# Kernel optimization log

Hardware: AMD Instinct MI355X
Metric: run time of the kernel (lower is better)

The kernel has to match this reference:

```python
import jax, jax.numpy as jnp
import numpy as np

B, Q, T, C = 2, 300, 25, 256
NH, NL, NP = 8, 4, 4
DFF = 1024
HD = C // NH
SHAPES = [(128, 128), (64, 64), (32, 32), (16, 16)]  # (H_l, W_l) per level
S = sum(h * w for h, w in SHAPES)
LQ = Q * T


def setup_inputs() -> dict:
    key = jax.random.key(0)
    ks = jax.random.split(key, 16)
    rn = lambda k, shape, s=0.02: jax.random.normal(k, shape, jnp.float32) * s
    starts = np.cumsum([0] + [h * w for h, w in SHAPES[:-1]])
    return {
        "tgt_text": jax.random.normal(ks[0], (B, Q, T, C), jnp.float32),
        "query_pos_text": jax.random.normal(ks[1], (B, Q, T, C), jnp.float32),
        "reference_points": jax.random.uniform(ks[2], (B, LQ, NL, 2), jnp.float32),
        "src": jax.random.normal(ks[3], (B, S, C), jnp.float32),
        "src_spatial_shapes": jnp.array(SHAPES, jnp.int32),
        "level_start_index": jnp.array(starts, jnp.int32),
        "in_proj_w": rn(ks[4], (3 * C, C)), "in_proj_b": jnp.zeros((3 * C,), jnp.float32),
        "out_proj_w": rn(ks[5], (C, C)), "out_proj_b": jnp.zeros((C,), jnp.float32),
        "ln1_g": jnp.ones((C,), jnp.float32), "ln1_b": jnp.zeros((C,), jnp.float32),
        "samp_off_w": rn(ks[6], (NH * NL * NP * 2, C)), "samp_off_b": rn(ks[7], (NH * NL * NP * 2,), 0.5),
        "aw_w": rn(ks[8], (NH * NL * NP, C)), "aw_b": jnp.zeros((NH * NL * NP,), jnp.float32),
        "vp_w": rn(ks[9], (C, C)), "vp_b": jnp.zeros((C,), jnp.float32),
        "op_w": rn(ks[10], (C, C)), "op_b": jnp.zeros((C,), jnp.float32),
        "ln2_g": jnp.ones((C,), jnp.float32), "ln2_b": jnp.zeros((C,), jnp.float32),
        "ffn1_w": rn(ks[11], (DFF, C)), "ffn1_b": jnp.zeros((DFF,), jnp.float32),
        "ffn2_w": rn(ks[12], (C, DFF)), "ffn2_b": jnp.zeros((C,), jnp.float32),
        "ln3_g": jnp.ones((C,), jnp.float32), "ln3_b": jnp.zeros((C,), jnp.float32),
    }


def _ln(x, g, b):
    m = jnp.mean(x, axis=-1, keepdims=True)
    v = jnp.var(x, axis=-1, keepdims=True)
    return (x - m) / jnp.sqrt(v + 1e-5) * g + b


def _self_attn(tgt, pos, in_proj_w, in_proj_b, out_proj_w, out_proj_b):
    # torch nn.MultiheadAttention math: q,k carry pos, v is raw tgt
    qk = (tgt + pos).reshape(B * Q, T, C)
    x = tgt.reshape(B * Q, T, C)
    Wq, Wk, Wv = jnp.split(in_proj_w, 3, axis=0)
    bq, bk, bv = jnp.split(in_proj_b, 3, axis=0)
    heads = lambda t: t.reshape(B * Q, T, NH, HD).transpose(0, 2, 1, 3)
    q = heads(qk @ Wq.T + bq)
    k = heads(qk @ Wk.T + bk)
    v = heads(x @ Wv.T + bv)
    attn = jax.nn.softmax(jnp.einsum("bhqd,bhkd->bhqk", q, k) / jnp.sqrt(jnp.float32(HD)), axis=-1)
    o = jnp.einsum("bhqk,bhkd->bhqd", attn, v).transpose(0, 2, 1, 3).reshape(B * Q, T, C)
    return (o @ out_proj_w.T + out_proj_b).reshape(B, Q, T, C)


def _ms_deform_attn(query, reference_points, src, shapes, samp_off_w, samp_off_b, aw_w, aw_b, vp_w, vp_b, op_w, op_b):
    # query: [B, LQ, C]; src: [B, S, C]
    value = (src @ vp_w.T + vp_b).reshape(B, S, NH, HD)
    off = (query @ samp_off_w.T + samp_off_b).reshape(B, LQ, NH, NL, NP, 2)
    aw = jax.nn.softmax((query @ aw_w.T + aw_b).reshape(B, LQ, NH, NL * NP), axis=-1)
    aw = aw.reshape(B, LQ, NH, NL, NP)
    # normalizer is (W_l, H_l)
    norm = jnp.array([[w, h] for (h, w) in shapes], jnp.float32)
    loc = reference_points[:, :, None, :, None, :] + off / norm[None, None, None, :, None, :]
    starts = np.cumsum([0] + [h * w for h, w in shapes])
    accum = jnp.zeros((B, NH, LQ, HD), jnp.float32)
    for l, (Hl, Wl) in enumerate(shapes):
        vl = value[:, starts[l]:starts[l] + Hl * Wl].transpose(0, 2, 1, 3)  # [B,NH,HW,HD]
        # grid_sample align_corners=False pixel coords
        xl = (loc[:, :, :, l, :, 0] * Wl - 0.5).transpose(0, 2, 1, 3).reshape(B, NH, LQ * NP)
        yl = (loc[:, :, :, l, :, 1] * Hl - 0.5).transpose(0, 2, 1, 3).reshape(B, NH, LQ * NP)
        x0 = jnp.floor(xl); y0 = jnp.floor(yl)
        wx1 = xl - x0; wy1 = yl - y0
        x0i = x0.astype(jnp.int32); y0i = y0.astype(jnp.int32)
        samp = jnp.zeros((B, NH, LQ * NP, HD), jnp.float32)
        for dx, dy, w in ((0, 0, (1 - wx1) * (1 - wy1)), (1, 0, wx1 * (1 - wy1)),
                          (0, 1, (1 - wx1) * wy1), (1, 1, wx1 * wy1)):
            xi = x0i + dx; yi = y0i + dy
            valid = (xi >= 0) & (xi < Wl) & (yi >= 0) & (yi < Hl)
            lin = jnp.clip(yi, 0, Hl - 1) * Wl + jnp.clip(xi, 0, Wl - 1)
            g = jnp.take_along_axis(vl, lin[..., None], axis=2)  # [B,NH,LQ*NP,HD]
            samp = samp + g * (w * valid)[..., None]
        samp = samp.reshape(B, NH, LQ, NP, HD)
        awl = aw[:, :, :, l, :].transpose(0, 2, 1, 3)  # [B,NH,LQ,NP]
        accum = accum + jnp.sum(samp * awl[..., None], axis=3)
    out = accum.transpose(0, 2, 1, 3).reshape(B, LQ, C)
    return out @ op_w.T + op_b


def reference(tgt_text, query_pos_text, reference_points, src, src_spatial_shapes, level_start_index,
              in_proj_w, in_proj_b, out_proj_w, out_proj_b, ln1_g, ln1_b,
              samp_off_w, samp_off_b, aw_w, aw_b, vp_w, vp_b, op_w, op_b, ln2_g, ln2_b,
              ffn1_w, ffn1_b, ffn2_w, ffn2_b, ln3_g, ln3_b):
    shapes = [tuple(int(v) for v in row) for row in np.asarray(src_spatial_shapes)]  # static
    # --- intra-text self-attention ---
    tgt2 = _self_attn(tgt_text, query_pos_text, in_proj_w, in_proj_b, out_proj_w, out_proj_b)
    tgt = _ln(tgt_text + tgt2, ln1_g, ln1_b)
    # --- multi-scale deformable cross-attention ---
    query = (tgt + query_pos_text).reshape(B, LQ, C)
    cross = _ms_deform_attn(query, reference_points, src, shapes,
                            samp_off_w, samp_off_b, aw_w, aw_b, vp_w, vp_b, op_w, op_b)
    tgt = _ln(tgt + cross.reshape(B, Q, T, C), ln2_g, ln2_b)
    # --- FFN ---
    ffn = jax.nn.relu(tgt @ ffn1_w.T + ffn1_b) @ ffn2_w.T + ffn2_b
    return _ln(tgt + ffn, ln3_g, ln3_b)
```

## Files before the change

kernel.cpp:

```cpp
#include <hip/hip_runtime.h>
#include <cstddef>

#define B_ 2
#define Q_ 300
#define T_ 25
#define C_ 256
#define NH_ 8
#define NL_ 4
#define NP_ 4
#define HD_ 32
#define DFF_ 1024
#define LQ_ (Q_ * T_)
#define NTOK_ (B_ * LQ_)
#define S_ 21760
#define BS_ (B_ * S_)

typedef __bf16 bf16x8 __attribute__((ext_vector_type(8)));
typedef float floatx4 __attribute__((ext_vector_type(4)));
typedef unsigned short ushort_t;

__device__ __forceinline__ unsigned pack_bf16(float x, float y) {
    unsigned ux = __float_as_uint(x) + 0x8000u;
    unsigned uy = __float_as_uint(y) + 0x8000u;
    return (ux >> 16) | (uy & 0xFFFF0000u);
}
__device__ __forceinline__ ushort_t f2bf_s(float x) {
    return (ushort_t)((__float_as_uint(x) + 0x8000u) >> 16);
}
__device__ __forceinline__ float bf2f(ushort_t u) {
    return __uint_as_float((unsigned)u << 16);
}

#define WOFF_IP   0
#define WOFF_OUT  196608
#define WOFF_VP   262144
#define WOFF_SO   327680
#define WOFF_AW   393216
#define WOFF_OP   425984
#define WOFF_F1   491520
#define WOFF_F2   753664
#define WTOTAL    1015808

__global__ __launch_bounds__(256) void convw_kernel(
    const float* __restrict__ ipw, const float* __restrict__ outw,
    const float* __restrict__ vpw, const float* __restrict__ sampw,
    const float* __restrict__ aww, const float* __restrict__ opw,
    const float* __restrict__ f1w, const float* __restrict__ f2w,
    ushort_t* __restrict__ dst)
{
    long long g = ((long long)blockIdx.x * 256 + threadIdx.x) * 8;
    if (g >= WTOTAL) return;
    const float* src; long long off;
    if      (g < WOFF_OUT) { src = ipw;   off = WOFF_IP; }
    else if (g < WOFF_VP)  { src = outw;  off = WOFF_OUT; }
    else if (g < WOFF_SO)  { src = vpw;   off = WOFF_VP; }
    else if (g < WOFF_AW)  { src = sampw; off = WOFF_SO; }
    else if (g < WOFF_OP)  { src = aww;   off = WOFF_AW; }
    else if (g < WOFF_F1)  { src = opw;   off = WOFF_OP; }
    else if (g < WOFF_F2)  { src = f1w;   off = WOFF_F1; }
    else                   { src = f2w;   off = WOFF_F2; }
    const float4* s4 = (const float4*)(src + (g - off));
    float4 a = s4[0], b = s4[1];
    uint4 o;
    o.x = pack_bf16(a.x, a.y); o.y = pack_bf16(a.z, a.w);
    o.z = pack_bf16(b.x, b.y); o.w = pack_bf16(b.z, b.w);
    *(uint4*)(dst + g) = o;
}

#define GBN 128
#define GBK 32
#define LDA_S 40

template<int AMODE, int OUTMODE, int GBMT>
__global__ __launch_bounds__(256) void gemm_w(
    const void* __restrict__ Av, const float* __restrict__ A2,
    const ushort_t* __restrict__ W,
    const float* __restrict__ bias, const float* __restrict__ bias2, int N1,
    void* __restrict__ Cv, long long partStride,
    int M, int N, int K, int kChunk, int ldc, int relu)
{
    constexpr int LA = GBMT / 32;
    constexpr int WM = GBMT / 2;
    constexpr int NI = WM / 16;

    __shared__ unsigned short Asl[GBMT * LDA_S];
    __shared__ unsigned short Bsl[GBN * LDA_S];

    const int m0 = blockIdx.x * GBMT;
    const int n0 = blockIdx.y * GBN;
    const int z  = blockIdx.z;
    const int kbeg = z * kChunk;
    const int kend = min(K, kbeg + kChunk);

    const int t  = threadIdx.x;
    const int wid  = t >> 6;
    const int lane = t & 63;
    const int wm = (wid >> 1) * WM;
    const int wn = (wid & 1) * 64;
    const int fm = lane & 15;
    const int fq = (lane >> 4) * 8;

    floatx4 acc[NI][4];
    #pragma unroll
    for (int i = 0; i < NI; ++i)
        #pragma unroll
        for (int j = 0; j < 4; ++j)
            acc[i][j] = (floatx4){0.f, 0.f, 0.f, 0.f};

    float4 pa[LA];
    uint2  pab[LA];
    uint2  pwb[4];
    const float* Af = (const float*)Av;
    const ushort_t* Ab = (const ushort_t*)Av;

    auto load_tiles = [&](int k0) {
        #pragma unroll
        for (int i = 0; i < LA; ++i) {
            int idx = t + 256 * i;
            int row = idx >> 3;
            int c4  = (idx & 7) * 4;
            int gm = m0 + row;
            if constexpr (AMODE == 2) {
                uint2 v = {0u, 0u};
                if (gm < M) v = *(const uint2*)(Ab + (size_t)gm * K + k0 + c4);
                pab[i] = v;
            } else {
                float4 v = make_float4(0.f, 0.f, 0.f, 0.f);
                if (gm < M) {
                    v = *(const float4*)(Af + (size_t)gm * K + k0 + c4);
                    if constexpr (AMODE == 1) {
                        float4 v2 = *(const float4*)(A2 + (size_t)gm * K + k0 + c4);
                        v.x += v2.x; v.y += v2.y; v.z += v2.z; v.w += v2.w;
                    }
                }
                pa[i] = v;
            }
        }
        #pragma unroll
        for (int i = 0; i < 4; ++i) {
            int idx = t + 256 * i;
            int row = idx >> 3;
            int c4  = (idx & 7) * 4;
            pwb[i] = *(const uint2*)(W + (size_t)(n0 + row) * K + k0 + c4);
        }
    };

    load_tiles(kbeg);
    for (int k0 = kbeg; k0 < kend; k0 += GBK) {
        #pragma unroll
        for (int i = 0; i < LA; ++i) {
            int idx = t + 256 * i;
            int row = idx >> 3;
            int c4  = (idx & 7) * 4;
            if constexpr (AMODE == 2) {
                *(uint2*)&Asl[row * LDA_S + c4] = pab[i];
            } else {
                uint2 p;
                p.x = pack_bf16(pa[i].x, pa[i].y);
                p.y = pack_bf16(pa[i].z, pa[i].w);
                *(uint2*)&Asl[row * LDA_S + c4] = p;
            }
        }
        #pragma unroll
        for (int i = 0; i < 4; ++i) {
            int idx = t + 256 * i;
            int row = idx >> 3;
            int c4  = (idx & 7) * 4;
            *(uint2*)&Bsl[row * LDA_S + c4] = pwb[i];
        }
        __syncthreads();

        if (k0 + GBK < kend) load_tiles(k0 + GBK);

        bf16x8 af[NI], bfr[4];
        #pragma unroll
        for (int i = 0; i < NI; ++i)
            af[i] = *(const bf16x8*)&Asl[(wm + i * 16 + fm) * LDA_S + fq];
        #pragma unroll
        for (int j = 0; j < 4; ++j)
            bfr[j] = *(const bf16x8*)&Bsl[(wn + j * 16 + fm) * LDA_S + fq];

        #pragma unroll
        for (int i = 0; i < NI; ++i)
            #pragma unroll
            for (int j = 0; j < 4; ++j)
                acc[i][j] = __builtin_amdgcn_mfma_f32_16x16x32_bf16(af[i], bfr[j], acc[i][j], 0, 0, 0);
        __syncthreads();
    }

    float* Cf = (float*)Cv + (long long)z * partStride;
    ushort_t* Cb = (ushort_t*)Cv;
    const int cr = (lane >> 4) * 4;
    const int cc = lane & 15;
    #pragma unroll
    for (int j = 0; j < 4; ++j) {
        int gn = n0 + wn + j * 16 + cc;
        float bia = 0.f;
        if (z == 0) bia = (bias2 && gn >= N1) ? bias2[gn - N1] : bias[gn];
        #pragma unroll
        for (int i = 0; i < NI; ++i) {
            #pragma unroll
            for (int r = 0; r < 4; ++r) {
                int gm = m0 + wm + i * 16 + cr + r;
                if (gm < M) {
                    float v = acc[i][j][r] + bia;
                    if (relu) v = fmaxf(v, 0.f);
                    if constexpr (OUTMODE == 2) {
                        int bb = gm >= S_;
                        int s  = gm - bb * S_;
                        Cb[(((size_t)(bb * 8 + (gn >> 5))) * S_ + s) * 32 + (gn & 31)] = f2bf_s(v);
                    } else if constexpr (OUTMODE == 1) {
                        Cb[(size_t)gm * ldc + gn] = f2bf_s(v);
                    } else {
                        Cf[(size_t)gm * ldc + gn] = v;
                    }
                }
            }
        }
    }
}

__global__ __launch_bounds__(64) void attn_kernel(
    const ushort_t* __restrict__ qkv,
    ushort_t* __restrict__ o)
{
    int sh = blockIdx.x;
    int s = sh >> 3, h = sh & 7;
    __shared__ float qs[T_][HD_], ks[T_][HD_], vs[T_][HD_];
    int t = threadIdx.x;

    for (int idx = t; idx < T_ * HD_; idx += 64) {
        int i = idx >> 5, d = idx & 31;
        size_t base = ((size_t)(s * T_ + i)) * 768 + h * HD_ + d;
        qs[i][d] = bf2f(qkv[base]);
        ks[i][d] = bf2f(qkv[base + 256]);
        vs[i][d] = bf2f(qkv[base + 512]);
    }
    __syncthreads();

    if (t < T_) {
        float sc[T_];
        float mx = -1e30f;
        #pragma unroll
        for (int j = 0; j < T_; ++j) {
            float dot = 0.f;
            #pragma unroll
            for (int d = 0; d < HD_; ++d) dot += qs[t][d] * ks[j][d];
            sc[j] = dot * 0.17677669529663687f;
            mx = fmaxf(mx, sc[j]);
        }
        float sum = 0.f;
        #pragma unroll
        for (int j = 0; j < T_; ++j) { sc[j] = __expf(sc[j] - mx); sum += sc[j]; }
        float inv = 1.f / sum;
        float out[HD_];
        #pragma unroll
        for (int d = 0; d < HD_; ++d) out[d] = 0.f;
        for (int j = 0; j < T_; ++j) {
            float p = sc[j] * inv;
            #pragma unroll
            for (int d = 0; d < HD_; ++d) out[d] += p * vs[j][d];
        }
        size_t ob = ((size_t)(s * T_ + t)) * C_ + h * HD_;
        #pragma unroll
        for (int d = 0; d < HD_; ++d) o[ob + d] = f2bf_s(out[d]);
    }
}

__global__ __launch_bounds__(256) void ln4_kernel(
    const float* __restrict__ x, const float* __restrict__ r,
    int nparts, long long rstride,
    const float* __restrict__ g, const float* __restrict__ b,
    float* __restrict__ out, const float* __restrict__ pos,
    float* __restrict__ qout)
{
    const int wave = threadIdx.x >> 6;
    const int lane = threadIdx.x & 63;
    const int tok = blockIdx.x * 4 + wave;
    const size_t base = (size_t)tok * C_ + lane * 4;

    float4 v = *(const float4*)(x + base);
    for (int p = 0; p < nparts; ++p) {
        float4 rv = *(const float4*)(r + base + (long long)p * rstride);
        v.x += rv.x; v.y += rv.y; v.z += rv.z; v.w += rv.w;
    }
    float s  = v.x + v.y + v.z + v.w;
    float ss = v.x * v.x + v.y * v.y + v.z * v.z + v.w * v.w;
    #pragma unroll
    for (int m = 32; m; m >>= 1) {
        s  += __shfl_xor(s, m);
        ss += __shfl_xor(ss, m);
    }
    float mean = s * (1.f / 256.f);
    float var  = ss * (1.f / 256.f) - mean * mean;
    float rstd = rsqrtf(var + 1e-5f);

    float4 gv = *(const float4*)(g + lane * 4);
    float4 bv = *(const float4*)(b + lane * 4);
    float4 y;
    y.x = (v.x - mean) * rstd * gv.x + bv.x;
    y.y = (v.y - mean) * rstd * gv.y + bv.y;
    y.z = (v.z - mean) * rstd * gv.z + bv.z;
    y.w = (v.w - mean) * rstd * gv.w + bv.w;
    *(float4*)(out + base) = y;
    if (qout) {
        float4 pv = *(const float4*)(pos + base);
        float4 q;
        q.x = y.x + pv.x; q.y = y.y + pv.y; q.z = y.z + pv.z; q.w = y.w + pv.w;
        *(float4*)(qout + base) = q;
    }
}

__global__ __launch_bounds__(256) void deform_kernel(
    const ushort_t* __restrict__ value,
    const float* __restrict__ d12,
    const float* __restrict__ refpts,
    ushort_t* __restrict__ out)
{
    const int lane = threadIdx.x & 63;
    const int wave = threadIdx.x >> 6;
    const int half = lane >> 5;
    const int tok = blockIdx.x * 8 + wave * 2 + half;
    const int h  = (lane >> 2) & 7;
    const int d8 = (lane & 3) * 8;
    const int b = tok / LQ_;

    const float* awp = d12 + (size_t)tok * 384 + 256 + h * 16;
    float logit[16];
    float mx = -1e30f;
    #pragma unroll
    for (int i = 0; i < 16; ++i) { logit[i] = awp[i]; mx = fmaxf(mx, logit[i]); }
    float sum = 0.f;
    #pragma unroll
    for (int i = 0; i < 16; ++i) { logit[i] = __expf(logit[i] - mx); sum += logit[i]; }
    float inv = 1.f / sum;

    const float* offp = d12 + (size_t)tok * 384 + h * 32;
    const float* refp = refpts + (size_t)tok * (NL_ * 2);

    const int HW[4]     = {128, 64, 32, 16};
    const int starts[4] = {0, 16384, 20480, 21504};

    float accv[8];
    #pragma unroll
    for (int i = 0; i < 8; ++i) accv[i] = 0.f;

    #pragma unroll
    for (int l = 0; l < 4; ++l) {
        const int Hl = HW[l], Wl = HW[l];
        float rx = refp[l * 2 + 0], ry = refp[l * 2 + 1];
        const ushort_t* vbase = value + (((size_t)(b * 8 + h)) * S_ + starts[l]) * HD_ + d8;
        #pragma unroll
        for (int p = 0; p < 4; ++p) {
            float ox = offp[(l * 4 + p) * 2 + 0];
            float oy = offp[(l * 4 + p) * 2 + 1];
            float xl = rx * (float)Wl + ox - 0.5f;
            float yl = ry * (float)Hl + oy - 0.5f;
            float x0f = floorf(xl), y0f = floorf(yl);
            int x0 = (int)x0f, y0 = (int)y0f;
            float wx1 = xl - x0f, wy1 = yl - y0f;
            float wx0 = 1.f - wx1, wy0 = 1.f - wy1;
            float aww = logit[l * 4 + p] * inv;

            #pragma unroll
            for (int c = 0; c < 4; ++c) {
                int dx = c & 1, dy = c >> 1;
                int xi = x0 + dx, yi = y0 + dy;
                float w = (dx ? wx1 : wx0) * (dy ? wy1 : wy0);
                bool valid = (xi >= 0) & (xi < Wl) & (yi >= 0) & (yi < Hl);
                int xc = min(max(xi, 0), Wl - 1);
                int yc = min(max(yi, 0), Hl - 1);
                float wc = (valid ? w : 0.f) * aww;
                uint4 raw = *(const uint4*)(vbase + (size_t)(yc * Wl + xc) * HD_);
                accv[0] += __uint_as_float((raw.x & 0xFFFFu) << 16) * wc;
                accv[1] += __uint_as_float(raw.x & 0xFFFF0000u) * wc;
                accv[2] += __uint_as_float((raw.y & 0xFFFFu) << 16) * wc;
                accv[3] += __uint_as_float(raw.y & 0xFFFF0000u) * wc;
                accv[4] += __uint_as_float((raw.z & 0xFFFFu) << 16) * wc;
                accv[5] += __uint_as_float(raw.z & 0xFFFF0000u) * wc;
                accv[6] += __uint_as_float((raw.w & 0xFFFFu) << 16) * wc;
                accv[7] += __uint_as_float(raw.w & 0xFFFF0000u) * wc;
            }
        }
    }
    uint4 po;
    po.x = pack_bf16(accv[0], accv[1]);
    po.y = pack_bf16(accv[2], accv[3]);
    po.z = pack_bf16(accv[4], accv[5]);
    po.w = pack_bf16(accv[6], accv[7]);
    *(uint4*)(out + (size_t)tok * C_ + h * HD_ + d8) = po;
}

extern "C" void kernel_launch(void* const* d_in, const int* in_sizes, int n_in,
                              void* d_out, int out_size, void* d_ws, size_t ws_size,
                              hipStream_t stream) {
    const float* tgt_text = (const float*)d_in[0];
    const float* pos      = (const float*)d_in[1];
    const float* refpts   = (const float*)d_in[2];
    const float* src      = (const float*)d_in[3];
    const float* in_proj_w  = (const float*)d_in[6];
    const float* in_proj_b  = (const float*)d_in[7];
    const float* out_proj_w = (const float*)d_in[8];
    const float* out_proj_b = (const float*)d_in[9];
    const float* ln1_g = (const float*)d_in[10];
    const float* ln1_b = (const float*)d_in[11];
    const float* samp_off_w = (const float*)d_in[12];
    const float* samp_off_b = (const float*)d_in[13];
    const float* aw_w = (const float*)d_in[14];
    const float* aw_b = (const float*)d_in[15];
    const float* vp_w = (const float*)d_in[16];
    const float* vp_b = (const float*)d_in[17];
    const float* op_w = (const float*)d_in[18];
    const float* op_b = (const float*)d_in[19];
    const float* ln2_g = (const float*)d_in[20];
    const float* ln2_b = (const float*)d_in[21];
    const float* ffn1_w = (const float*)d_in[22];
    const float* ffn1_b = (const float*)d_in[23];
    const float* ffn2_w = (const float*)d_in[24];
    const float* ffn2_b = (const float*)d_in[25];
    const float* ln3_g = (const float*)d_in[26];
    const float* ln3_b = (const float*)d_in[27];

    const long long NC = (long long)NTOK_ * C_;
    float* ws = (float*)d_ws;
    float* A    = ws;
    float* Bq   = ws + NC;
    float* Creg = ws + 2 * NC;
    float* D12  = Creg + (long long)NTOK_ * DFF_;
    float* E    = D12 + (long long)NTOK_ * 384;
    float* F    = E + NC;
    ushort_t* wb = (ushort_t*)(F + NC);

    ushort_t* qkv  = (ushort_t*)Creg;
    ushort_t* valt = (ushort_t*)Creg + (size_t)NTOK_ * 768;

    const int MB64  = (NTOK_ + 63) / 64;
    const int MB128 = (NTOK_ + 127) / 128;
    const int MBV64 = BS_ / 64;

    convw_kernel<<<496, 256, 0, stream>>>(in_proj_w, out_proj_w, vp_w, samp_off_w,
                                          aw_w, op_w, ffn1_w, ffn2_w, wb);
    gemm_w<1, 1, 64><<<dim3(MB64, 4, 1), 256, 0, stream>>>(tgt_text, pos, wb + WOFF_IP,
        in_proj_b, nullptr, 0, qkv, 0, NTOK_, 512, 256, 256, 768, 0);
    gemm_w<0, 1, 64><<<dim3(MB64, 2, 1), 256, 0, stream>>>(tgt_text, nullptr, wb + WOFF_IP + 512 * 256,
        in_proj_b + 512, nullptr, 0, qkv + 512, 0, NTOK_, 256, 256, 256, 768, 0);
    gemm_w<0, 2, 64><<<dim3(MBV64, 2, 1), 256, 0, stream>>>(src, nullptr, wb + WOFF_VP,
        vp_b, nullptr, 0, valt, 0, BS_, 256, 256, 256, 0, 0);
    attn_kernel<<<B_ * Q_ * NH_, 64, 0, stream>>>(qkv, (ushort_t*)E);
    gemm_w<2, 0, 64><<<dim3(MB64, 2, 1), 256, 0, stream>>>(E, nullptr, wb + WOFF_OUT,
        out_proj_b, nullptr, 0, F, 0, NTOK_, 256, 256, 256, 256, 0);
    ln4_kernel<<<NTOK_ / 4, 256, 0, stream>>>(tgt_text, F, 1, 0,
                                              ln1_g, ln1_b, A, pos, Bq);
    gemm_w<0, 0, 64><<<dim3(MB64, 3, 1), 256, 0, stream>>>(Bq, nullptr, wb + WOFF_SO,
        samp_off_b, aw_b, 256, D12, 0, NTOK_, 384, 256, 256, 384, 0);
    deform_kernel<<<NTOK_ / 8, 256, 0, stream>>>(valt, D12, refpts, (ushort_t*)E);
    gemm_w<2, 0, 64><<<dim3(MB64, 2, 1), 256, 0, stream>>>(E, nullptr, wb + WOFF_OP,
        op_b, nullptr, 0, F, 0, NTOK_, 256, 256, 256, 256, 0);
    ln4_kernel<<<NTOK_ / 4, 256, 0, stream>>>(A, F, 1, 0,
                                              ln2_g, ln2_b, A, nullptr, nullptr);
    gemm_w<0, 1, 128><<<dim3(MB128, 8, 1), 256, 0, stream>>>(A, nullptr, wb + WOFF_F1,
        ffn1_b, nullptr, 0, Creg, 0, NTOK_, DFF_, 256, 256, DFF_, 1);
    gemm_w<2, 0, 64><<<dim3(MB64, 2, 2), 256, 0, stream>>>(Creg, nullptr, wb + WOFF_F2,
        ffn2_b, nullptr, 0, E, NC, NTOK_, 256, 1024, 512, 256, 0);
    ln4_kernel<<<NTOK_ / 4, 256, 0, stream>>>(A, E, 2, NC,
                                              ln3_g, ln3_b, (float*)d_out, nullptr, nullptr);
}
```

Baseline: 436.3 us.

## Remap deform blocks per (batch,head) plane for XCD locality; merge QKV GEMMs

The deformable sampling kernel now assigns each block one head of one batch and a chunk of 64 tokens. The block index is decoded so that every block sharing a value plane lands on the same XCD, which keeps each plane's gathers inside one L2. Single-use loads of offsets, logits and reference points become nontemporal so they do not evict value data. The two input-projection GEMMs are merged into one launch, with the positional add applied only to the Q/K column blocks via a runtime flag. This adds one branch per A load.

```diff
diff --git a/kernel.cpp b/kernel.cpp
--- a/kernel.cpp
+++ b/kernel.cpp
@@ -100,6 +100,8 @@
     const int fm = lane & 15;
     const int fq = (lane >> 4) * 8;
 
+    const bool addA2 = (AMODE == 1) && (n0 < N1);
+
     floatx4 acc[NI][4];
     #pragma unroll
     for (int i = 0; i < NI; ++i)
@@ -129,8 +131,10 @@
                 if (gm < M) {
                     v = *(const float4*)(Af + (size_t)gm * K + k0 + c4);
                     if constexpr (AMODE == 1) {
-                        float4 v2 = *(const float4*)(A2 + (size_t)gm * K + k0 + c4);
-                        v.x += v2.x; v.y += v2.y; v.z += v2.z; v.w += v2.w;
+                        if (addA2) {
+                            float4 v2 = *(const float4*)(A2 + (size_t)gm * K + k0 + c4);
+                            v.x += v2.x; v.y += v2.y; v.z += v2.z; v.w += v2.w;
+                        }
                     }
                 }
                 pa[i] = v;
@@ -311,25 +315,38 @@
     }
 }
 
+#define DCHUNK_ 118
 __global__ __launch_bounds__(256) void deform_kernel(
     const ushort_t* __restrict__ value,
     const float* __restrict__ d12,
     const float* __restrict__ refpts,
     ushort_t* __restrict__ out)
 {
+    const int bi    = blockIdx.x;
+    const int xcd   = bi & 7;
+    const int yy    = bi >> 3;
+    const int combo = xcd + 8 * (yy & 1);
+    const int chunk = yy >> 1;
+    const int h     = combo & 7;
+
+    const int wave = threadIdx.x >> 6;
     const int lane = threadIdx.x & 63;
-    const int wave = threadIdx.x >> 6;
-    const int half = lane >> 5;
-    const int tok = blockIdx.x * 8 + wave * 2 + half;
-    const int h  = (lane >> 2) & 7;
-    const int d8 = (lane & 3) * 8;
-    const int b = tok / LQ_;
+    const int ti   = lane >> 2;
+    const int d8   = (lane & 3) * 8;
+
+    int tl = chunk * 64 + wave * 16 + ti;
+    const bool active = (tl < LQ_);
+    tl = min(tl, LQ_ - 1);
+    const int tok = (combo >> 3) * LQ_ + tl;
 
     const float* awp = d12 + (size_t)tok * 384 + 256 + h * 16;
     float logit[16];
     float mx = -1e30f;
     #pragma unroll
-    for (int i = 0; i < 16; ++i) { logit[i] = awp[i]; mx = fmaxf(mx, logit[i]); }
+    for (int i = 0; i < 16; ++i) {
+        logit[i] = __builtin_nontemporal_load(awp + i);
+        mx = fmaxf(mx, logit[i]);
+    }
     float sum = 0.f;
     #pragma unroll
     for (int i = 0; i < 16; ++i) { logit[i] = __expf(logit[i] - mx); sum += logit[i]; }
@@ -341,6 +358,8 @@
     const int HW[4]     = {128, 64, 32, 16};
     const int starts[4] = {0, 16384, 20480, 21504};
 
+    const ushort_t* vplane = value + (size_t)combo * ((size_t)S_ * HD_) + d8;
+
     float accv[8];
     #pragma unroll
     for (int i = 0; i < 8; ++i) accv[i] = 0.f;
@@ -348,12 +367,13 @@
     #pragma unroll
     for (int l = 0; l < 4; ++l) {
         const int Hl = HW[l], Wl = HW[l];
-        float rx = refp[l * 2 + 0], ry = refp[l * 2 + 1];
-        const ushort_t* vbase = value + (((size_t)(b * 8 + h)) * S_ + starts[l]) * HD_ + d8;
+        float rx = __builtin_nontemporal_load(refp + l * 2 + 0);
+        float ry = __builtin_nontemporal_load(refp + l * 2 + 1);
+        const ushort_t* vbase = vplane + (size_t)starts[l] * HD_;
         #pragma unroll
         for (int p = 0; p < 4; ++p) {
-            float ox = offp[(l * 4 + p) * 2 + 0];
-            float oy = offp[(l * 4 + p) * 2 + 1];
+            float ox = __builtin_nontemporal_load(offp + (l * 4 + p) * 2 + 0);
+            float oy = __builtin_nontemporal_load(offp + (l * 4 + p) * 2 + 1);
             float xl = rx * (float)Wl + ox - 0.5f;
             float yl = ry * (float)Hl + oy - 0.5f;
             float x0f = floorf(xl), y0f = floorf(yl);
@@ -383,12 +403,14 @@
             }
         }
     }
-    uint4 po;
-    po.x = pack_bf16(accv[0], accv[1]);
-    po.y = pack_bf16(accv[2], accv[3]);
-    po.z = pack_bf16(accv[4], accv[5]);
-    po.w = pack_bf16(accv[6], accv[7]);
-    *(uint4*)(out + (size_t)tok * C_ + h * HD_ + d8) = po;
+    if (active) {
+        uint4 po;
+        po.x = pack_bf16(accv[0], accv[1]);
+        po.y = pack_bf16(accv[2], accv[3]);
+        po.z = pack_bf16(accv[4], accv[5]);
+        po.w = pack_bf16(accv[6], accv[7]);
+        *(uint4*)(out + (size_t)tok * C_ + h * HD_ + d8) = po;
+    }
 }
 
 extern "C" void kernel_launch(void* const* d_in, const int* in_sizes, int n_in,
@@ -440,10 +462,8 @@
 
     convw_kernel<<<496, 256, 0, stream>>>(in_proj_w, out_proj_w, vp_w, samp_off_w,
                                           aw_w, op_w, ffn1_w, ffn2_w, wb);
-    gemm_w<1, 1, 64><<<dim3(MB64, 4, 1), 256, 0, stream>>>(tgt_text, pos, wb + WOFF_IP,
-        in_proj_b, nullptr, 0, qkv, 0, NTOK_, 512, 256, 256, 768, 0);
-    gemm_w<0, 1, 64><<<dim3(MB64, 2, 1), 256, 0, stream>>>(tgt_text, nullptr, wb + WOFF_IP + 512 * 256,
-        in_proj_b + 512, nullptr, 0, qkv + 512, 0, NTOK_, 256, 256, 256, 768, 0);
+    gemm_w<1, 1, 64><<<dim3(MB64, 6, 1), 256, 0, stream>>>(tgt_text, pos, wb + WOFF_IP,
+        in_proj_b, nullptr, 512, qkv, 0, NTOK_, 768, 256, 256, 768, 0);
     gemm_w<0, 2, 64><<<dim3(MBV64, 2, 1), 256, 0, stream>>>(src, nullptr, wb + WOFF_VP,
         vp_b, nullptr, 0, valt, 0, BS_, 256, 256, 256, 0, 0);
     attn_kernel<<<B_ * Q_ * NH_, 64, 0, stream>>>(qkv, (ushort_t*)E);
@@ -453,7 +473,7 @@
                                               ln1_g, ln1_b, A, pos, Bq);
     gemm_w<0, 0, 64><<<dim3(MB64, 3, 1), 256, 0, stream>>>(Bq, nullptr, wb + WOFF_SO,
         samp_off_b, aw_b, 256, D12, 0, NTOK_, 384, 256, 256, 384, 0);
-    deform_kernel<<<NTOK_ / 8, 256, 0, stream>>>(valt, D12, refpts, (ushort_t*)E);
+    deform_kernel<<<8 * 2 * DCHUNK_, 256, 0, stream>>>(valt, D12, refpts, (ushort_t*)E);
     gemm_w<2, 0, 64><<<dim3(MB64, 2, 1), 256, 0, stream>>>(E, nullptr, wb + WOFF_OP,
         op_b, nullptr, 0, F, 0, NTOK_, 256, 256, 256, 256, 0);
     ln4_kernel<<<NTOK_ / 4, 256, 0, stream>>>(A, F, 1, 0,
```

New measurement: 426.2 us. -2.3%, faster.
